# Performance work log

Hardware: AMD Instinct MI355X
Metric: run time of the kernel (lower is better)

Reference implementation:

```python
import jax, jax.numpy as jnp
import numpy as np

GH, GW, B, H, OUT = 9, 9, 1024, 256, 1


def setup_inputs() -> dict:
    key = jax.random.key(0)
    ks = jax.random.split(key, 16)
    N = GH * GW
    s3 = 1.0 / np.sqrt(3 * H)
    sH = 1.0 / np.sqrt(H)
    return {
        "x": jax.random.normal(ks[0], (B, GH, GW), jnp.float32),
        "h_ext": jax.random.normal(ks[1], (B, H), jnp.float32),
        "c_ext": jax.random.normal(ks[2], (B, H), jnp.float32),
        "grid_h": jax.random.normal(ks[3], (GH, GW, B, H), jnp.float32),
        "grid_c": jax.random.normal(ks[4], (GH, GW, B, H), jnp.float32),
        "W_hp": jax.random.normal(ks[5], (N, H, 3 * H), jnp.float32) * s3,
        "b_hp": jax.random.normal(ks[6], (N, H), jnp.float32) * s3,
        "W_cp": jax.random.normal(ks[7], (N, H, 3 * H), jnp.float32) * s3,
        "b_cp": jax.random.normal(ks[8], (N, H), jnp.float32) * s3,
        "W_ih": jax.random.normal(ks[9], (N, 4 * H, 1), jnp.float32) * sH,
        "W_hh": jax.random.normal(ks[10], (N, 4 * H, H), jnp.float32) * sH,
        "b_ih": jax.random.normal(ks[11], (N, 4 * H), jnp.float32) * sH,
        "b_hh": jax.random.normal(ks[12], (N, 4 * H), jnp.float32) * sH,
        "W_out": jax.random.normal(ks[13], (OUT, H), jnp.float32) * sH,
        "b_out": jnp.zeros((OUT,), jnp.float32),
    }


def _lstm_cell(x_cell, h0, c0, W_ih_k, W_hh_k, b_ih_k, b_hh_k):
    # x_cell: [B,1], h0/c0: [B,H]; torch LSTMCell math
    gates = x_cell @ W_ih_k.T + b_ih_k + h0 @ W_hh_k.T + b_hh_k  # [B,4H]
    i, f, g, o = jnp.split(gates, 4, axis=1)
    i, f, o = jax.nn.sigmoid(i), jax.nn.sigmoid(f), jax.nn.sigmoid(o)
    g = jnp.tanh(g)
    c = f * c0 + i * g
    h = o * jnp.tanh(c)
    return h, c


def reference(x, h_ext, c_ext, grid_h, grid_c,
              W_hp, b_hp, W_cp, b_cp,
              W_ih, W_hh, b_ih, b_hh, W_out, b_out):
    zeros = jnp.zeros((B, H), x.dtype)
    # new states, updated in raster order; left/up neighbors read NEW states
    new_h = [[None] * GW for _ in range(GH)]
    new_c = [[None] * GW for _ in range(GH)]
    for i in range(GH):
        for j in range(GW):
            k = i * GW + j
            h_prev, c_prev = grid_h[i, j], grid_c[i, j]
            if i == 0 and j == 0:
                h_left, c_left = h_ext, c_ext
            elif j > 0:
                h_left, c_left = new_h[i][j - 1], new_c[i][j - 1]
            else:
                h_left, c_left = zeros, zeros
            if i > 0:
                h_up, c_up = new_h[i - 1][j], new_c[i - 1][j]
            else:
                h_up, c_up = zeros, zeros
            comb_h = jnp.concatenate([h_left, h_up, h_prev], axis=1)  # [B,3H]
            comb_c = jnp.concatenate([c_left, c_up, c_prev], axis=1)
            ph = comb_h @ W_hp[k].T + b_hp[k]
            pc = comb_c @ W_cp[k].T + b_cp[k]
            x_cell = x[:, i, j][:, None]  # [B,1]
            h_new, c_new = _lstm_cell(x_cell, ph, pc, W_ih[k], W_hh[k], b_ih[k], b_hh[k])
            new_h[i][j], new_c[i][j] = h_new, c_new
    final_h, final_c = new_h[-1][-1], new_c[-1][-1]
    # fc_out with fc_layers_out=[0]: Linear + ReLU, then sigmoid
    out = jax.nn.sigmoid(jax.nn.relu(final_h @ W_out.T + b_out))
    gh = jnp.stack([jnp.stack(r, 0) for r in new_h], 0)
    gc = jnp.stack([jnp.stack(r, 0) for r in new_c], 0)
    return out, final_h, final_c, gh, gc
```

## Files before the change

### kernel.cpp

```cpp
#include <hip/hip_runtime.h>
#include <math.h>

#define BATCH 1024
#define HID 256
#define W3 768
#define SLOT (BATCH * HID)

typedef __bf16 bf16_t;
typedef __bf16 bf16x8 __attribute__((ext_vector_type(8)));
typedef __bf16 bf16x4 __attribute__((ext_vector_type(4)));
typedef float f32x4 __attribute__((ext_vector_type(4)));

__device__ inline bf16x8 cvt8(const float4 a, const float4 b) {
    bf16x8 r;
    r[0] = (bf16_t)a.x; r[1] = (bf16_t)a.y; r[2] = (bf16_t)a.z; r[3] = (bf16_t)a.w;
    r[4] = (bf16_t)b.x; r[5] = (bf16_t)b.y; r[6] = (bf16_t)b.z; r[7] = (bf16_t)b.w;
    return r;
}
__device__ inline bf16x4 cvt4(const float4 a) {
    bf16x4 r;
    r[0] = (bf16_t)a.x; r[1] = (bf16_t)a.y; r[2] = (bf16_t)a.z; r[3] = (bf16_t)a.w;
    return r;
}

template<bool ATOMIC>
__device__ __forceinline__ void proj_core(
        const float* __restrict__ src, const float* __restrict__ W, int koff,
        const float* __restrict__ bias, float* __restrict__ out,
        bf16_t (*Asm)[40], bf16_t (*Bsm)[40]) {
    const int t = threadIdx.x;
    const int lane = t & 63, wid = t >> 6;
    const int wm = wid & 1, wn = wid >> 1;
    const int ln = lane & 15, lh = lane >> 4;
    const int b0 = blockIdx.x * 128, n0 = blockIdx.y * 128;
    const int sr = t >> 1, sq = (t & 1) * 16;
    const float* arow = src + (size_t)(b0 + sr) * HID + sq;
    const float* wrow = W + (size_t)(n0 + sr) * W3 + koff + sq;
    f32x4 acc[4][4] = {};
    for (int kb = 0; kb < 8; ++kb) {
        const float4 a0 = *(const float4*)(arow + kb * 32);
        const float4 a1 = *(const float4*)(arow + kb * 32 + 4);
        const float4 a2 = *(const float4*)(arow + kb * 32 + 8);
        const float4 a3 = *(const float4*)(arow + kb * 32 + 12);
        const float4 w0 = *(const float4*)(wrow + kb * 32);
        const float4 w1 = *(const float4*)(wrow + kb * 32 + 4);
        const float4 w2 = *(const float4*)(wrow + kb * 32 + 8);
        const float4 w3 = *(const float4*)(wrow + kb * 32 + 12);
        const bf16x8 av0 = cvt8(a0, a1), av1 = cvt8(a2, a3);
        const bf16x8 bv0 = cvt8(w0, w1), bv1 = cvt8(w2, w3);
        __syncthreads();
        *(bf16x8*)&Asm[sr][sq] = av0;
        *(bf16x8*)&Asm[sr][sq + 8] = av1;
        *(bf16x8*)&Bsm[sr][sq] = bv0;
        *(bf16x8*)&Bsm[sr][sq + 8] = bv1;
        __syncthreads();
        bf16x8 af[4], bfv[4];
        #pragma unroll
        for (int mf = 0; mf < 4; ++mf)
            af[mf] = *(const bf16x8*)&Asm[wm * 64 + mf * 16 + ln][lh * 8];
        #pragma unroll
        for (int nf = 0; nf < 4; ++nf)
            bfv[nf] = *(const bf16x8*)&Bsm[wn * 64 + nf * 16 + ln][lh * 8];
        #pragma unroll
        for (int mf = 0; mf < 4; ++mf)
            #pragma unroll
            for (int nf = 0; nf < 4; ++nf)
                acc[mf][nf] = __builtin_amdgcn_mfma_f32_16x16x32_bf16(
                    af[mf], bfv[nf], acc[mf][nf], 0, 0, 0);
    }
    #pragma unroll
    for (int nf = 0; nf < 4; ++nf) {
        const int n = n0 + wn * 64 + nf * 16 + ln;
        const float bn = ATOMIC ? 0.f : bias[n];
        #pragma unroll
        for (int mf = 0; mf < 4; ++mf)
            #pragma unroll
            for (int r = 0; r < 4; ++r) {
                const int b = b0 + wm * 64 + mf * 16 + lh * 4 + r;
                if (ATOMIC)
                    unsafeAtomicAdd(out + (size_t)b * HID + n, acc[mf][nf][r]);
                else
                    out[(size_t)b * HID + n] = acc[mf][nf][r] + bn;
            }
    }
}

__global__ __launch_bounds__(256) void baseproj_kernel(
        const float* __restrict__ gridh, const float* __restrict__ gridc,
        const float* __restrict__ Whp, const float* __restrict__ Wcp,
        const float* __restrict__ bhp, const float* __restrict__ bcp,
        float* __restrict__ phb, float* __restrict__ pcb) {
    __shared__ bf16_t As[128][40];
    __shared__ bf16_t Bs[128][40];
    const int z = blockIdx.z, k = z >> 1, hc = z & 1;
    const float* src = (hc ? gridc : gridh) + (size_t)k * SLOT;
    const float* W = (hc ? Wcp : Whp) + (size_t)k * HID * W3;
    const float* bias = (hc ? bcp : bhp) + (size_t)k * HID;
    float* out = (hc ? pcb : phb) + (size_t)k * SLOT;
    proj_core<false>(src, W, 512, bias, out, As, Bs);
}

__global__ __launch_bounds__(256) void gatesbase_kernel(
        const float* __restrict__ phb, const float* __restrict__ Whh,
        const float* __restrict__ Wih, const float* __restrict__ bih,
        const float* __restrict__ bhh, const float* __restrict__ x,
        float* __restrict__ gbase) {
    __shared__ bf16_t As[128][40];
    __shared__ bf16_t Bs[128][40];
    const int k = blockIdx.z;
    const int t = threadIdx.x;
    const int lane = t & 63, wid = t >> 6;
    const int wm = wid & 1, wn = wid >> 1;
    const int ln = lane & 15, lh = lane >> 4;
    const int b0 = blockIdx.x * 128;
    const int ub = blockIdx.y, u0 = ub * 32;
    const int sr = t >> 1, sq = (t & 1) * 16;
    const float* arow = phb + (size_t)k * SLOT + (size_t)(b0 + sr) * HID + sq;
    const int g_r = sr >> 5, du_r = sr & 31;
    const float* wrow = Whh + (size_t)k * 4 * HID * HID
                        + (size_t)(g_r * HID + u0 + du_r) * HID + sq;
    f32x4 acc[4][4] = {};
    for (int kb = 0; kb < 8; ++kb) {
        const float4 a0 = *(const float4*)(arow + kb * 32);
        const float4 a1 = *(const float4*)(arow + kb * 32 + 4);
        const float4 a2 = *(const float4*)(arow + kb * 32 + 8);
        const float4 a3 = *(const float4*)(arow + kb * 32 + 12);
        const float4 w0 = *(const float4*)(wrow + kb * 32);
        const float4 w1 = *(const float4*)(wrow + kb * 32 + 4);
        const float4 w2 = *(const float4*)(wrow + kb * 32 + 8);
        const float4 w3 = *(const float4*)(wrow + kb * 32 + 12);
        const bf16x8 av0 = cvt8(a0, a1), av1 = cvt8(a2, a3);
        const bf16x8 bv0 = cvt8(w0, w1), bv1 = cvt8(w2, w3);
        __syncthreads();
        *(bf16x8*)&As[sr][sq] = av0;
        *(bf16x8*)&As[sr][sq + 8] = av1;
        *(bf16x8*)&Bs[sr][sq] = bv0;
        *(bf16x8*)&Bs[sr][sq + 8] = bv1;
        __syncthreads();
        bf16x8 af[4], bfr[4];
        #pragma unroll
        for (int mf = 0; mf < 4; ++mf)
            af[mf] = *(const bf16x8*)&As[wm * 64 + mf * 16 + ln][lh * 8];
        #pragma unroll
        for (int g = 0; g < 4; ++g)
            bfr[g] = *(const bf16x8*)&Bs[g * 32 + wn * 16 + ln][lh * 8];
        #pragma unroll
        for (int mf = 0; mf < 4; ++mf)
            #pragma unroll
            for (int g = 0; g < 4; ++g)
                acc[mf][g] = __builtin_amdgcn_mfma_f32_16x16x32_bf16(
                    af[mf], bfr[g], acc[mf][g], 0, 0, 0);
    }
    const int u = u0 + wn * 16 + ln;
    float wih[4], bb[4];
    #pragma unroll
    for (int g = 0; g < 4; ++g) {
        const int n4 = g * HID + u;
        wih[g] = Wih[(size_t)k * 4 * HID + n4];
        bb[g] = bih[(size_t)k * 4 * HID + n4] + bhh[(size_t)k * 4 * HID + n4];
    }
    float* orow = gbase + (size_t)k * BATCH * 1024;
    #pragma unroll
    for (int mf = 0; mf < 4; ++mf)
        #pragma unroll
        for (int r = 0; r < 4; ++r) {
            const int b = b0 + wm * 64 + mf * 16 + lh * 4 + r;
            const float xv = x[(size_t)b * 81 + k];
            #pragma unroll
            for (int g = 0; g < 4; ++g)
                orow[(size_t)b * 1024 + ub * 128 + g * 32 + wn * 16 + ln] =
                    acc[mf][g][r] + xv * wih[g] + bb[g],
                (void)0;
            #pragma unroll
            for (int g = 1; g < 4; ++g) { }
        }
}

__global__ __launch_bounds__(256) void compose_kernel(
        const float* __restrict__ Whh, const float* __restrict__ Whp,
        bf16_t* __restrict__ CC) {
    __shared__ bf16_t As[128][40];
    __shared__ bf16_t Bs[128][40];
    const int k = blockIdx.z;
    const int t = threadIdx.x;
    const int lane = t & 63, wid = t >> 6;
    const int wm = wid & 1, wn = wid >> 1;
    const int ln = lane & 15, lh = lane >> 4;
    const int m0 = blockIdx.x * 128;
    const int by = blockIdx.y;
    const int sr = t >> 1, sq = (t & 1) * 16;
    const int g_r = sr >> 5, du_r = sr & 31;
    const float* arow = Whh + (size_t)k * 4 * HID * HID
                        + (size_t)(g_r * HID + by * 32 + du_r) * HID + sq;
    const float* wbase = Whp + (size_t)k * HID * W3;
    const int uu = t >> 3, mm0 = (t & 7) * 16;
    f32x4 acc[4][4] = {};
    for (int kb = 0; kb < 8; ++kb) {
        const float4 a0 = *(const float4*)(arow + kb * 32);
        const float4 a1 = *(const float4*)(arow + kb * 32 + 4);
        const float4 a2 = *(const float4*)(arow + kb * 32 + 8);
        const float4 a3 = *(const float4*)(arow + kb * 32 + 12);
        const float* bsrc = wbase + (size_t)(kb * 32 + uu) * W3 + m0 + mm0;
        const float4 v0 = *(const float4*)(bsrc);
        const float4 v1 = *(const float4*)(bsrc + 4);
        const float4 v2 = *(const float4*)(bsrc + 8);
        const float4 v3 = *(const float4*)(bsrc + 12);
        const bf16x8 av0 = cvt8(a0, a1), av1 = cvt8(a2, a3);
        const bf16x4 bq[4] = { cvt4(v0), cvt4(v1), cvt4(v2), cvt4(v3) };
        __syncthreads();
        *(bf16x8*)&As[sr][sq] = av0;
        *(bf16x8*)&As[sr][sq + 8] = av1;
        #pragma unroll
        for (int q = 0; q < 4; ++q)
            #pragma unroll
            for (int e = 0; e < 4; ++e)
                Bs[mm0 + q * 4 + e][uu] = bq[q][e];
        __syncthreads();
        bf16x8 af[4], bf[4];
        #pragma unroll
        for (int mf = 0; mf < 4; ++mf)
            af[mf] = *(const bf16x8*)&As[wm * 64 + mf * 16 + ln][lh * 8];
        #pragma unroll
        for (int nf = 0; nf < 4; ++nf)
            bf[nf] = *(const bf16x8*)&Bs[wn * 64 + nf * 16 + ln][lh * 8];
        #pragma unroll
        for (int mf = 0; mf < 4; ++mf)
            #pragma unroll
            for (int nf = 0; nf < 4; ++nf)
                acc[mf][nf] = __builtin_amdgcn_mfma_f32_16x16x32_bf16(
                    af[mf], bf[nf], acc[mf][nf], 0, 0, 0);
    }
    bf16_t* out = CC + (size_t)k * 1024 * 512;
    #pragma unroll
    for (int nf = 0; nf < 4; ++nf) {
        const int m = m0 + wn * 64 + nf * 16 + ln;
        #pragma unroll
        for (int mf = 0; mf < 4; ++mf)
            #pragma unroll
            for (int r = 0; r < 4; ++r) {
                const int c = by * 128 + wm * 64 + mf * 16 + lh * 4 + r;
                out[(size_t)c * 512 + m] = (bf16_t)acc[mf][nf][r];
            }
    }
}

struct FusedDesc {
    const float* hl; const float* cl;
    const float* hu; const float* cu;
    const float* gb;
    const float* pcb;
    const bf16_t* cc;
    const float* wcp;
    float* gh; float* gc;
};
struct FusedBatchArgs { FusedDesc d[9]; };

__global__ __launch_bounds__(256) void fused_kernel(FusedBatchArgs args) {
    const FusedDesc fd = args.d[blockIdx.z];
    __shared__ bf16_t A1[128][40];
    __shared__ bf16_t A2[128][40];
    __shared__ bf16_t B1[128][40];
    __shared__ bf16_t B2[32][40];
    const int t = threadIdx.x;
    const int lane = t & 63, wid = t >> 6;
    const int wm = wid & 1, wn = wid >> 1;
    const int ln = lane & 15, lh = lane >> 4;
    const int b0 = blockIdx.x * 128;
    const int by = blockIdx.y, u0 = by * 32;
    const int sr = t >> 1, sq = (t & 1) * 16;
    const int du2 = t >> 3, kk4 = (t & 7) * 4;

    const float* hs[2]; const float* cs[2]; int ko[2]; int ns = 0;
    if (fd.hl) { hs[ns] = fd.hl; cs[ns] = fd.cl; ko[ns] = 0;   ++ns; }
    if (fd.hu) { hs[ns] = fd.hu; cs[ns] = fd.cu; ko[ns] = 256; ++ns; }

    f32x4 accg[4][4] = {};
    f32x4 accp[4] = {};

    for (int s = 0; s < ns; ++s) {
        const float* ha = hs[s] + (size_t)(b0 + sr) * HID + sq;
        const float* ca = cs[s] + (size_t)(b0 + sr) * HID + sq;
        const bf16_t* b1r = fd.cc + (size_t)(by * 128 + sr) * 512 + ko[s] + sq;
        const float* b2r = fd.wcp + (size_t)(u0 + du2) * W3 + ko[s] + kk4;
        for (int kb = 0; kb < 8; ++kb) {
            const float4 h0 = *(const float4*)(ha + kb * 32);
            const float4 h1 = *(const float4*)(ha + kb * 32 + 4);
            const float4 h2 = *(const float4*)(ha + kb * 32 + 8);
            const float4 h3 = *(const float4*)(ha + kb * 32 + 12);
            const float4 c0 = *(const float4*)(ca + kb * 32);
            const float4 c1 = *(const float4*)(ca + kb * 32 + 4);
            const float4 c2 = *(const float4*)(ca + kb * 32 + 8);
            const float4 c3 = *(const float4*)(ca + kb * 32 + 12);
            const bf16x8 w0 = *(const bf16x8*)(b1r + kb * 32);
            const bf16x8 w1 = *(const bf16x8*)(b1r + kb * 32 + 8);
            const float4 p0 = *(const float4*)(b2r + kb * 32);
            const bf16x8 hv0 = cvt8(h0, h1), hv1 = cvt8(h2, h3);
            const bf16x8 cv0 = cvt8(c0, c1), cv1 = cvt8(c2, c3);
            const bf16x4 pv = cvt4(p0);
            __syncthreads();
            *(bf16x8*)&A1[sr][sq] = hv0;
            *(bf16x8*)&A1[sr][sq + 8] = hv1;
            *(bf16x8*)&A2[sr][sq] = cv0;
            *(bf16x8*)&A2[sr][sq + 8] = cv1;
            *(bf16x8*)&B1[sr][sq] = w0;
            *(bf16x8*)&B1[sr][sq + 8] = w1;
            *(bf16x4*)&B2[du2][kk4] = pv;
            __syncthreads();
            bf16x8 af1[4], bf1[4], af2[4], bf2;
            #pragma unroll
            for (int mf = 0; mf < 4; ++mf) {
                af1[mf] = *(const bf16x8*)&A1[wm * 64 + mf * 16 + ln][lh * 8];
                af2[mf] = *(const bf16x8*)&A2[wm * 64 + mf * 16 + ln][lh * 8];
            }
            #pragma unroll
            for (int g = 0; g < 4; ++g)
                bf1[g] = *(const bf16x8*)&B1[g * 32 + wn * 16 + ln][lh * 8];
            bf2 = *(const bf16x8*)&B2[wn * 16 + ln][lh * 8];
            #pragma unroll
            for (int mf = 0; mf < 4; ++mf) {
                #pragma unroll
                for (int g = 0; g < 4; ++g)
                    accg[mf][g] = __builtin_amdgcn_mfma_f32_16x16x32_bf16(
                        af1[mf], bf1[g], accg[mf][g], 0, 0, 0);
                accp[mf] = __builtin_amdgcn_mfma_f32_16x16x32_bf16(
                    af2[mf], bf2, accp[mf], 0, 0, 0);
            }
        }
    }

    const int u = u0 + wn * 16 + ln;
    #pragma unroll
    for (int mf = 0; mf < 4; ++mf)
        #pragma unroll
        for (int r = 0; r < 4; ++r) {
            const int b = b0 + wm * 64 + mf * 16 + lh * 4 + r;
            const float* gbr = fd.gb + (size_t)b * 1024 + by * 128 + wn * 16 + ln;
            const float gi = accg[mf][0][r] + gbr[0];
            const float gf = accg[mf][1][r] + gbr[32];
            const float gg = accg[mf][2][r] + gbr[64];
            const float go = accg[mf][3][r] + gbr[96];
            const float pc = accp[mf][r] + fd.pcb[(size_t)b * HID + u];
            const float i_ = 1.f / (1.f + expf(-gi));
            const float f_ = 1.f / (1.f + expf(-gf));
            const float o_ = 1.f / (1.f + expf(-go));
            const float g_ = tanhf(gg);
            const float cn = f_ * pc + i_ * g_;
            const float hn = o_ * tanhf(cn);
            fd.gh[(size_t)b * HID + u] = hn;
            fd.gc[(size_t)b * HID + u] = cn;
        }
}

struct SegDesc { const float* src; const float* W; const float* bias; float* out; int koff; };
struct SegArgs { SegDesc d[36]; };

__global__ __launch_bounds__(256) void projseg_kernel(SegArgs a) {
    __shared__ bf16_t As[128][40];
    __shared__ bf16_t Bs[128][40];
    const SegDesc d = a.d[blockIdx.z];
    if (d.bias) proj_core<false>(d.src, d.W, d.koff, d.bias, d.out, As, Bs);
    else        proj_core<true>(d.src, d.W, d.koff, nullptr, d.out, As, Bs);
}

struct CellDesc {
    const float* ph; const float* pc;
    const float* Whh; const float* Wih; const float* bih; const float* bhh;
    const float* xcol;
    float* gh; float* gc;
};
struct CellBatchArgs { CellDesc d[9]; };

__global__ __launch_bounds__(256) void cell_kernel(CellBatchArgs args) {
    const CellDesc cd = args.d[blockIdx.z];
    __shared__ bf16_t Psm[128][40];
    __shared__ bf16_t Wsm[128][40];
    const int t = threadIdx.x;
    const int lane = t & 63, wid = t >> 6;
    const int wm = wid & 1, wn = wid >> 1;
    const int ln = lane & 15, lh = lane >> 4;
    const int b0 = blockIdx.x * 128;
    const int u0 = blockIdx.y * 32;
    const int sr = t >> 1, sq = (t & 1) * 16;
    const float* prow = cd.ph + (size_t)(b0 + sr) * HID + sq;
    const int cg = sr >> 5, cdu = sr & 31;
    const float* wrow = cd.Whh + (size_t)(cg * HID + u0 + cdu) * HID + sq;
    f32x4 acc[4][4] = {};
    for (int kb = 0; kb < 8; ++kb) {
        const float4 p0 = *(const float4*)(prow + kb * 32);
        const float4 p1 = *(const float4*)(prow + kb * 32 + 4);
        const float4 p2 = *(const float4*)(prow + kb * 32 + 8);
        const float4 p3 = *(const float4*)(prow + kb * 32 + 12);
        const float4 w0 = *(const float4*)(wrow + kb * 32);
        const float4 w1 = *(const float4*)(wrow + kb * 32 + 4);
        const float4 w2 = *(const float4*)(wrow + kb * 32 + 8);
        const float4 w3 = *(const float4*)(wrow + kb * 32 + 12);
        const bf16x8 pv0 = cvt8(p0, p1), pv1 = cvt8(p2, p3);
        const bf16x8 wv0 = cvt8(w0, w1), wv1 = cvt8(w2, w3);
        __syncthreads();
        *(bf16x8*)&Psm[sr][sq] = pv0;
        *(bf16x8*)&Psm[sr][sq + 8] = pv1;
        *(bf16x8*)&Wsm[sr][sq] = wv0;
        *(bf16x8*)&Wsm[sr][sq + 8] = wv1;
        __syncthreads();
        bf16x8 af[4], bfr[4];
        #pragma unroll
        for (int mf = 0; mf < 4; ++mf)
            af[mf] = *(const bf16x8*)&Psm[wm * 64 + mf * 16 + ln][lh * 8];
        #pragma unroll
        for (int g = 0; g < 4; ++g)
            bfr[g] = *(const bf16x8*)&Wsm[g * 32 + wn * 16 + ln][lh * 8];
        #pragma unroll
        for (int mf = 0; mf < 4; ++mf)
            #pragma unroll
            for (int g = 0; g < 4; ++g)
                acc[mf][g] = __builtin_amdgcn_mfma_f32_16x16x32_bf16(
                    af[mf], bfr[g], acc[mf][g], 0, 0, 0);
    }
    const int u = u0 + wn * 16 + ln;
    float wih[4], bsum[4];
    #pragma unroll
    for (int g = 0; g < 4; ++g) {
        const int n = g * HID + u;
        wih[g] = cd.Wih[n];
        bsum[g] = cd.bih[n] + cd.bhh[n];
    }
    #pragma unroll
    for (int mf = 0; mf < 4; ++mf)
        #pragma unroll
        for (int r = 0; r < 4; ++r) {
            const int b = b0 + wm * 64 + mf * 16 + lh * 4 + r;
            const float xv = cd.xcol[(size_t)b * 81];
            const float gi = acc[mf][0][r] + xv * wih[0] + bsum[0];
            const float gf = acc[mf][1][r] + xv * wih[1] + bsum[1];
            const float gg = acc[mf][2][r] + xv * wih[2] + bsum[2];
            const float go = acc[mf][3][r] + xv * wih[3] + bsum[3];
            const float i_ = 1.f / (1.f + expf(-gi));
            const float f_ = 1.f / (1.f + expf(-gf));
            const float o_ = 1.f / (1.f + expf(-go));
            const float g_ = tanhf(gg);
            const float c0 = cd.pc[(size_t)b * HID + u];
            const float cn = f_ * c0 + i_ * g_;
            const float hn = o_ * tanhf(cn);
            cd.gh[(size_t)b * HID + u] = hn;
            cd.gc[(size_t)b * HID + u] = cn;
        }
}

__global__ __launch_bounds__(256) void final_kernel(
        const float* __restrict__ gh88, const float* __restrict__ gc88,
        const float* __restrict__ Wout, const float* __restrict__ bout,
        float* __restrict__ out, float* __restrict__ fh, float* __restrict__ fc) {
    const int tid = blockIdx.x * blockDim.x + threadIdx.x;
    const int nth = gridDim.x * blockDim.x;
    for (int idx = tid; idx < BATCH * HID; idx += nth) {
        fh[idx] = gh88[idx];
        fc[idx] = gc88[idx];
    }
    if (tid < BATCH) {
        float s = bout[0];
        for (int k = 0; k < HID; ++k) s += gh88[(size_t)tid * HID + k] * Wout[k];
        s = fmaxf(s, 0.f);
        out[tid] = 1.f / (1.f + expf(-s));
    }
}

extern "C" void kernel_launch(void* const* d_in, const int* in_sizes, int n_in,
                              void* d_out, int out_size, void* d_ws, size_t ws_size,
                              hipStream_t stream) {
    const float* x      = (const float*)d_in[0];
    const float* h_ext  = (const float*)d_in[1];
    const float* c_ext  = (const float*)d_in[2];
    const float* grid_h = (const float*)d_in[3];
    const float* grid_c = (const float*)d_in[4];
    const float* W_hp   = (const float*)d_in[5];
    const float* b_hp   = (const float*)d_in[6];
    const float* W_cp   = (const float*)d_in[7];
    const float* b_cp   = (const float*)d_in[8];
    const float* W_ih   = (const float*)d_in[9];
    const float* W_hh   = (const float*)d_in[10];
    const float* b_ih   = (const float*)d_in[11];
    const float* b_hh   = (const float*)d_in[12];
    const float* W_out  = (const float*)d_in[13];
    const float* b_out  = (const float*)d_in[14];

    float* out = (float*)d_out;
    float* fh  = out + BATCH * 1;
    float* fc  = fh + SLOT;
    float* gh  = fc + SLOT;
    float* gc  = gh + (size_t)81 * SLOT;

    const size_t gb_bytes = (size_t)81 * BATCH * 1024 * 4;
    const size_t cc_bytes = (size_t)81 * 1024 * 512 * 2;
    const size_t pb_bytes = (size_t)81 * SLOT * 4;
    const size_t need_new = gb_bytes + cc_bytes + 2 * pb_bytes;

    if (ws_size >= need_new) {
        float* gbase = (float*)d_ws;
        bf16_t* CC = (bf16_t*)((char*)d_ws + gb_bytes);
        float* pcb = (float*)((char*)d_ws + gb_bytes + cc_bytes);
        float* phb = (float*)((char*)d_ws + gb_bytes + cc_bytes + pb_bytes);

        baseproj_kernel<<<dim3(8, 2, 162), 256, 0, stream>>>(
            grid_h, grid_c, W_hp, W_cp, b_hp, b_cp, phb, pcb);
        compose_kernel<<<dim3(4, 8, 81), 256, 0, stream>>>(W_hh, W_hp, CC);
        gatesbase_kernel<<<dim3(8, 8, 81), 256, 0, stream>>>(
            phb, W_hh, W_ih, b_ih, b_hh, x, gbase);

        for (int d = 0; d <= 16; ++d) {
            const int i_lo = d > 8 ? d - 8 : 0;
            const int i_hi = d < 8 ? d : 8;
            const int nc = i_hi - i_lo + 1;
            FusedBatchArgs fa{};
            for (int s = 0; s < nc; ++s) {
                const int i = i_lo + s, j = d - i;
                const int k = i * 9 + j;
                const float *hl = nullptr, *cl = nullptr, *hu = nullptr, *cu = nullptr;
                if (i == 0 && j == 0)      { hl = h_ext; cl = c_ext; }
                else if (j > 0)            { hl = gh + (size_t)(k - 1) * SLOT;
                                             cl = gc + (size_t)(k - 1) * SLOT; }
                if (i > 0)                 { hu = gh + (size_t)(k - 9) * SLOT;
                                             cu = gc + (size_t)(k - 9) * SLOT; }
                fa.d[s] = { hl, cl, hu, cu,
                            gbase + (size_t)k * BATCH * 1024,
                            pcb + (size_t)k * SLOT,
                            CC + (size_t)k * 1024 * 512,
                            W_cp + (size_t)k * HID * W3,
                            gh + (size_t)k * SLOT,
                            gc + (size_t)k * SLOT };
            }
            fused_kernel<<<dim3(8, 8, nc), 256, 0, stream>>>(fa);
        }
    } else {
        float* ws = (float*)d_ws;
        for (int d = 0; d <= 16; ++d) {
            const int i_lo = d > 8 ? d - 8 : 0;
            const int i_hi = d < 8 ? d : 8;
            const int nc = i_hi - i_lo + 1;
            SegArgs base{}, inc{};
            CellBatchArgs ca{};
            int nb = 0, ni = 0;
            for (int s = 0; s < nc; ++s) {
                const int i = i_lo + s, j = d - i;
                const int k = i * 9 + j;
                float* oh = ws + (size_t)(2 * s) * SLOT;
                float* oc = oh + SLOT;
                const float* Wh = W_hp + (size_t)k * HID * W3;
                const float* Wc = W_cp + (size_t)k * HID * W3;
                base.d[nb++] = { grid_h + (size_t)k * SLOT, Wh, b_hp + (size_t)k * HID, oh, 512 };
                base.d[nb++] = { grid_c + (size_t)k * SLOT, Wc, b_cp + (size_t)k * HID, oc, 512 };
                if (i == 0 && j == 0) {
                    inc.d[ni++] = { h_ext, Wh, nullptr, oh, 0 };
                    inc.d[ni++] = { c_ext, Wc, nullptr, oc, 0 };
                } else if (j > 0) {
                    inc.d[ni++] = { gh + (size_t)(k - 1) * SLOT, Wh, nullptr, oh, 0 };
                    inc.d[ni++] = { gc + (size_t)(k - 1) * SLOT, Wc, nullptr, oc, 0 };
                }
                if (i > 0) {
                    inc.d[ni++] = { gh + (size_t)(k - 9) * SLOT, Wh, nullptr, oh, 256 };
                    inc.d[ni++] = { gc + (size_t)(k - 9) * SLOT, Wc, nullptr, oc, 256 };
                }
                ca.d[s] = { oh, oc,
                            W_hh + (size_t)k * 4 * HID * HID,
                            W_ih + (size_t)k * 4 * HID,
                            b_ih + (size_t)k * 4 * HID,
                            b_hh + (size_t)k * 4 * HID,
                            x + i * 9 + j,
                            gh + (size_t)k * SLOT,
                            gc + (size_t)k * SLOT };
            }
            projseg_kernel<<<dim3(8, 2, nb), 256, 0, stream>>>(base);
            projseg_kernel<<<dim3(8, 2, ni), 256, 0, stream>>>(inc);
            cell_kernel<<<dim3(8, 8, nc), 256, 0, stream>>>(ca);
        }
    }
    final_kernel<<<dim3(64), 256, 0, stream>>>(
        gh + (size_t)80 * SLOT, gc + (size_t)80 * SLOT,
        W_out, b_out, out, fh, fc);
}
```

Before: 1.241 ms.

## Fold grid-state projection into wavefront stage kernel, drop precomputed gate buffers

Removes the separate base-projection and gates-base precompute kernels and their large fp32 workspace buffers. The composed Whh·Whp matrix is extended to cover all three input segments, so each stage kernel multiplies left, up and prior grid states directly. A small kernel folds Whh·b_hp and the LSTM biases into a per-cell gate vector, and x·W_ih is added in the epilogue. This cuts memory traffic for the gate-base and pc-base buffers, at the cost of the serial wavefront stages doing a third K-segment of work.

New measurement: 1.229 ms. Within noise of the previous version (-1.0%).

```diff
diff --git a/kernel.cpp b/kernel.cpp
--- a/kernel.cpp
+++ b/kernel.cpp
@@ -21,159 +21,6 @@
     bf16x4 r;
     r[0] = (bf16_t)a.x; r[1] = (bf16_t)a.y; r[2] = (bf16_t)a.z; r[3] = (bf16_t)a.w;
     return r;
-}
-
-template<bool ATOMIC>
-__device__ __forceinline__ void proj_core(
-        const float* __restrict__ src, const float* __restrict__ W, int koff,
-        const float* __restrict__ bias, float* __restrict__ out,
-        bf16_t (*Asm)[40], bf16_t (*Bsm)[40]) {
-    const int t = threadIdx.x;
-    const int lane = t & 63, wid = t >> 6;
-    const int wm = wid & 1, wn = wid >> 1;
-    const int ln = lane & 15, lh = lane >> 4;
-    const int b0 = blockIdx.x * 128, n0 = blockIdx.y * 128;
-    const int sr = t >> 1, sq = (t & 1) * 16;
-    const float* arow = src + (size_t)(b0 + sr) * HID + sq;
-    const float* wrow = W + (size_t)(n0 + sr) * W3 + koff + sq;
-    f32x4 acc[4][4] = {};
-    for (int kb = 0; kb < 8; ++kb) {
-        const float4 a0 = *(const float4*)(arow + kb * 32);
-        const float4 a1 = *(const float4*)(arow + kb * 32 + 4);
-        const float4 a2 = *(const float4*)(arow + kb * 32 + 8);
-        const float4 a3 = *(const float4*)(arow + kb * 32 + 12);
-        const float4 w0 = *(const float4*)(wrow + kb * 32);
-        const float4 w1 = *(const float4*)(wrow + kb * 32 + 4);
-        const float4 w2 = *(const float4*)(wrow + kb * 32 + 8);
-        const float4 w3 = *(const float4*)(wrow + kb * 32 + 12);
-        const bf16x8 av0 = cvt8(a0, a1), av1 = cvt8(a2, a3);
-        const bf16x8 bv0 = cvt8(w0, w1), bv1 = cvt8(w2, w3);
-        __syncthreads();
-        *(bf16x8*)&Asm[sr][sq] = av0;
-        *(bf16x8*)&Asm[sr][sq + 8] = av1;
-        *(bf16x8*)&Bsm[sr][sq] = bv0;
-        *(bf16x8*)&Bsm[sr][sq + 8] = bv1;
-        __syncthreads();
-        bf16x8 af[4], bfv[4];
-        #pragma unroll
-        for (int mf = 0; mf < 4; ++mf)
-            af[mf] = *(const bf16x8*)&Asm[wm * 64 + mf * 16 + ln][lh * 8];
-        #pragma unroll
-        for (int nf = 0; nf < 4; ++nf)
-            bfv[nf] = *(const bf16x8*)&Bsm[wn * 64 + nf * 16 + ln][lh * 8];
-        #pragma unroll
-        for (int mf = 0; mf < 4; ++mf)
-            #pragma unroll
-            for (int nf = 0; nf < 4; ++nf)
-                acc[mf][nf] = __builtin_amdgcn_mfma_f32_16x16x32_bf16(
-                    af[mf], bfv[nf], acc[mf][nf], 0, 0, 0);
-    }
-    #pragma unroll
-    for (int nf = 0; nf < 4; ++nf) {
-        const int n = n0 + wn * 64 + nf * 16 + ln;
-        const float bn = ATOMIC ? 0.f : bias[n];
-        #pragma unroll
-        for (int mf = 0; mf < 4; ++mf)
-            #pragma unroll
-            for (int r = 0; r < 4; ++r) {
-                const int b = b0 + wm * 64 + mf * 16 + lh * 4 + r;
-                if (ATOMIC)
-                    unsafeAtomicAdd(out + (size_t)b * HID + n, acc[mf][nf][r]);
-                else
-                    out[(size_t)b * HID + n] = acc[mf][nf][r] + bn;
-            }
-    }
-}
-
-__global__ __launch_bounds__(256) void baseproj_kernel(
-        const float* __restrict__ gridh, const float* __restrict__ gridc,
-        const float* __restrict__ Whp, const float* __restrict__ Wcp,
-        const float* __restrict__ bhp, const float* __restrict__ bcp,
-        float* __restrict__ phb, float* __restrict__ pcb) {
-    __shared__ bf16_t As[128][40];
-    __shared__ bf16_t Bs[128][40];
-    const int z = blockIdx.z, k = z >> 1, hc = z & 1;
-    const float* src = (hc ? gridc : gridh) + (size_t)k * SLOT;
-    const float* W = (hc ? Wcp : Whp) + (size_t)k * HID * W3;
-    const float* bias = (hc ? bcp : bhp) + (size_t)k * HID;
-    float* out = (hc ? pcb : phb) + (size_t)k * SLOT;
-    proj_core<false>(src, W, 512, bias, out, As, Bs);
-}
-
-__global__ __launch_bounds__(256) void gatesbase_kernel(
-        const float* __restrict__ phb, const float* __restrict__ Whh,
-        const float* __restrict__ Wih, const float* __restrict__ bih,
-        const float* __restrict__ bhh, const float* __restrict__ x,
-        float* __restrict__ gbase) {
-    __shared__ bf16_t As[128][40];
-    __shared__ bf16_t Bs[128][40];
-    const int k = blockIdx.z;
-    const int t = threadIdx.x;
-    const int lane = t & 63, wid = t >> 6;
-    const int wm = wid & 1, wn = wid >> 1;
-    const int ln = lane & 15, lh = lane >> 4;
-    const int b0 = blockIdx.x * 128;
-    const int ub = blockIdx.y, u0 = ub * 32;
-    const int sr = t >> 1, sq = (t & 1) * 16;
-    const float* arow = phb + (size_t)k * SLOT + (size_t)(b0 + sr) * HID + sq;
-    const int g_r = sr >> 5, du_r = sr & 31;
-    const float* wrow = Whh + (size_t)k * 4 * HID * HID
-                        + (size_t)(g_r * HID + u0 + du_r) * HID + sq;
-    f32x4 acc[4][4] = {};
-    for (int kb = 0; kb < 8; ++kb) {
-        const float4 a0 = *(const float4*)(arow + kb * 32);
-        const float4 a1 = *(const float4*)(arow + kb * 32 + 4);
-        const float4 a2 = *(const float4*)(arow + kb * 32 + 8);
-        const float4 a3 = *(const float4*)(arow + kb * 32 + 12);
-        const float4 w0 = *(const float4*)(wrow + kb * 32);
-        const float4 w1 = *(const float4*)(wrow + kb * 32 + 4);
-        const float4 w2 = *(const float4*)(wrow + kb * 32 + 8);
-        const float4 w3 = *(const float4*)(wrow + kb * 32 + 12);
-        const bf16x8 av0 = cvt8(a0, a1), av1 = cvt8(a2, a3);
-        const bf16x8 bv0 = cvt8(w0, w1), bv1 = cvt8(w2, w3);
-        __syncthreads();
-        *(bf16x8*)&As[sr][sq] = av0;
-        *(bf16x8*)&As[sr][sq + 8] = av1;
-        *(bf16x8*)&Bs[sr][sq] = bv0;
-        *(bf16x8*)&Bs[sr][sq + 8] = bv1;
-        __syncthreads();
-        bf16x8 af[4], bfr[4];
-        #pragma unroll
-        for (int mf = 0; mf < 4; ++mf)
-            af[mf] = *(const bf16x8*)&As[wm * 64 + mf * 16 + ln][lh * 8];
-        #pragma unroll
-        for (int g = 0; g < 4; ++g)
-            bfr[g] = *(const bf16x8*)&Bs[g * 32 + wn * 16 + ln][lh * 8];
-        #pragma unroll
-        for (int mf = 0; mf < 4; ++mf)
-            #pragma unroll
-            for (int g = 0; g < 4; ++g)
-                acc[mf][g] = __builtin_amdgcn_mfma_f32_16x16x32_bf16(
-                    af[mf], bfr[g], acc[mf][g], 0, 0, 0);
-    }
-    const int u = u0 + wn * 16 + ln;
-    float wih[4], bb[4];
-    #pragma unroll
-    for (int g = 0; g < 4; ++g) {
-        const int n4 = g * HID + u;
-        wih[g] = Wih[(size_t)k * 4 * HID + n4];
-        bb[g] = bih[(size_t)k * 4 * HID + n4] + bhh[(size_t)k * 4 * HID + n4];
-    }
-    float* orow = gbase + (size_t)k * BATCH * 1024;
-    #pragma unroll
-    for (int mf = 0; mf < 4; ++mf)
-        #pragma unroll
-        for (int r = 0; r < 4; ++r) {
-            const int b = b0 + wm * 64 + mf * 16 + lh * 4 + r;
-            const float xv = x[(size_t)b * 81 + k];
-            #pragma unroll
-            for (int g = 0; g < 4; ++g)
-                orow[(size_t)b * 1024 + ub * 128 + g * 32 + wn * 16 + ln] =
-                    acc[mf][g][r] + xv * wih[g] + bb[g],
-                (void)0;
-            #pragma unroll
-            for (int g = 1; g < 4; ++g) { }
-        }
 }
 
 __global__ __launch_bounds__(256) void compose_kernel(
@@ -216,21 +63,21 @@
             for (int e = 0; e < 4; ++e)
                 Bs[mm0 + q * 4 + e][uu] = bq[q][e];
         __syncthreads();
-        bf16x8 af[4], bf[4];
+        bf16x8 af[4], bfv[4];
         #pragma unroll
         for (int mf = 0; mf < 4; ++mf)
             af[mf] = *(const bf16x8*)&As[wm * 64 + mf * 16 + ln][lh * 8];
         #pragma unroll
         for (int nf = 0; nf < 4; ++nf)
-            bf[nf] = *(const bf16x8*)&Bs[wn * 64 + nf * 16 + ln][lh * 8];
+            bfv[nf] = *(const bf16x8*)&Bs[wn * 64 + nf * 16 + ln][lh * 8];
         #pragma unroll
         for (int mf = 0; mf < 4; ++mf)
             #pragma unroll
             for (int nf = 0; nf < 4; ++nf)
                 acc[mf][nf] = __builtin_amdgcn_mfma_f32_16x16x32_bf16(
-                    af[mf], bf[nf], acc[mf][nf], 0, 0, 0);
-    }
-    bf16_t* out = CC + (size_t)k * 1024 * 512;
+                    af[mf], bfv[nf], acc[mf][nf], 0, 0, 0);
+    }
+    bf16_t* outp = CC + (size_t)k * 1024 * W3;
     #pragma unroll
     for (int nf = 0; nf < 4; ++nf) {
         const int m = m0 + wn * 64 + nf * 16 + ln;
@@ -239,24 +86,49 @@
             #pragma unroll
             for (int r = 0; r < 4; ++r) {
                 const int c = by * 128 + wm * 64 + mf * 16 + lh * 4 + r;
-                out[(size_t)c * 512 + m] = (bf16_t)acc[mf][nf][r];
+                outp[(size_t)c * W3 + m] = (bf16_t)acc[mf][nf][r];
             }
     }
 }
 
-struct FusedDesc {
-    const float* hl; const float* cl;
-    const float* hu; const float* cu;
-    const float* gb;
-    const float* pcb;
+__global__ __launch_bounds__(256) void gvec_kernel(
+        const float* __restrict__ Whh, const float* __restrict__ bhp,
+        const float* __restrict__ bih, const float* __restrict__ bhh,
+        float* __restrict__ gvec) {
+    const int k = blockIdx.x, t = threadIdx.x;
+    __shared__ float bsm[HID];
+    bsm[t] = bhp[(size_t)k * HID + t];
+    __syncthreads();
+    #pragma unroll
+    for (int g = 0; g < 4; ++g) {
+        const int n4 = g * HID + t;
+        const float* wr = Whh + (size_t)k * 4 * HID * HID + (size_t)n4 * HID;
+        float s = 0.f;
+        for (int u = 0; u < HID; u += 4) {
+            const float4 w = *(const float4*)(wr + u);
+            s += w.x * bsm[u] + w.y * bsm[u + 1] + w.z * bsm[u + 2] + w.w * bsm[u + 3];
+        }
+        gvec[(size_t)k * 1024 + n4] = s + bih[(size_t)k * 1024 + n4]
+                                        + bhh[(size_t)k * 1024 + n4];
+    }
+}
+
+struct StageDesc {
+    const float* hs0; const float* cs0;
+    const float* hs1; const float* cs1;
+    const float* hs2; const float* cs2;
     const bf16_t* cc;
     const float* wcp;
+    const float* gvec;
+    const float* wih;
+    const float* bcp;
+    const float* xk;
     float* gh; float* gc;
 };
-struct FusedBatchArgs { FusedDesc d[9]; };
-
-__global__ __launch_bounds__(256) void fused_kernel(FusedBatchArgs args) {
-    const FusedDesc fd = args.d[blockIdx.z];
+struct StageArgs { StageDesc d[9]; };
+
+__global__ __launch_bounds__(256) void stage_kernel(StageArgs args) {
+    const StageDesc sd = args.d[blockIdx.z];
     __shared__ bf16_t A1[128][40];
     __shared__ bf16_t A2[128][40];
     __shared__ bf16_t B1[128][40];
@@ -270,18 +142,19 @@
     const int sr = t >> 1, sq = (t & 1) * 16;
     const int du2 = t >> 3, kk4 = (t & 7) * 4;
 
-    const float* hs[2]; const float* cs[2]; int ko[2]; int ns = 0;
-    if (fd.hl) { hs[ns] = fd.hl; cs[ns] = fd.cl; ko[ns] = 0;   ++ns; }
-    if (fd.hu) { hs[ns] = fd.hu; cs[ns] = fd.cu; ko[ns] = 256; ++ns; }
+    const float* hs[3] = { sd.hs0, sd.hs1, sd.hs2 };
+    const float* cs[3] = { sd.cs0, sd.cs1, sd.cs2 };
 
     f32x4 accg[4][4] = {};
     f32x4 accp[4] = {};
 
-    for (int s = 0; s < ns; ++s) {
+    for (int s = 0; s < 3; ++s) {
+        if (!hs[s]) continue;
+        const int ko = s * 256;
         const float* ha = hs[s] + (size_t)(b0 + sr) * HID + sq;
         const float* ca = cs[s] + (size_t)(b0 + sr) * HID + sq;
-        const bf16_t* b1r = fd.cc + (size_t)(by * 128 + sr) * 512 + ko[s] + sq;
-        const float* b2r = fd.wcp + (size_t)(u0 + du2) * W3 + ko[s] + kk4;
+        const bf16_t* b1r = sd.cc + (size_t)(by * 128 + sr) * W3 + ko + sq;
+        const float* b2r = sd.wcp + (size_t)(u0 + du2) * W3 + ko + kk4;
         for (int kb = 0; kb < 8; ++kb) {
             const float4 h0 = *(const float4*)(ha + kb * 32);
             const float4 h1 = *(const float4*)(ha + kb * 32 + 4);
@@ -306,7 +179,7 @@
             *(bf16x8*)&B1[sr][sq + 8] = w1;
             *(bf16x4*)&B2[du2][kk4] = pv;
             __syncthreads();
-            bf16x8 af1[4], bf1[4], af2[4], bf2;
+            bf16x8 af1[4], af2[4], bf1[4], bf2;
             #pragma unroll
             for (int mf = 0; mf < 4; ++mf) {
                 af1[mf] = *(const bf16x8*)&A1[wm * 64 + mf * 16 + ln][lh * 8];
@@ -329,26 +202,114 @@
     }
 
     const int u = u0 + wn * 16 + ln;
+    float wih[4], gv[4];
+    #pragma unroll
+    for (int g = 0; g < 4; ++g) {
+        const int n4 = g * HID + u;
+        wih[g] = sd.wih[n4];
+        gv[g] = sd.gvec[n4];
+    }
+    const float bc = sd.bcp[u];
     #pragma unroll
     for (int mf = 0; mf < 4; ++mf)
         #pragma unroll
         for (int r = 0; r < 4; ++r) {
             const int b = b0 + wm * 64 + mf * 16 + lh * 4 + r;
-            const float* gbr = fd.gb + (size_t)b * 1024 + by * 128 + wn * 16 + ln;
-            const float gi = accg[mf][0][r] + gbr[0];
-            const float gf = accg[mf][1][r] + gbr[32];
-            const float gg = accg[mf][2][r] + gbr[64];
-            const float go = accg[mf][3][r] + gbr[96];
-            const float pc = accp[mf][r] + fd.pcb[(size_t)b * HID + u];
+            const float xv = sd.xk[(size_t)b * 81];
+            const float gi = accg[mf][0][r] + gv[0] + xv * wih[0];
+            const float gf = accg[mf][1][r] + gv[1] + xv * wih[1];
+            const float gg = accg[mf][2][r] + gv[2] + xv * wih[2];
+            const float go = accg[mf][3][r] + gv[3] + xv * wih[3];
+            const float pc = accp[mf][r] + bc;
             const float i_ = 1.f / (1.f + expf(-gi));
             const float f_ = 1.f / (1.f + expf(-gf));
             const float o_ = 1.f / (1.f + expf(-go));
             const float g_ = tanhf(gg);
             const float cn = f_ * pc + i_ * g_;
             const float hn = o_ * tanhf(cn);
-            fd.gh[(size_t)b * HID + u] = hn;
-            fd.gc[(size_t)b * HID + u] = cn;
+            sd.gh[(size_t)b * HID + u] = hn;
+            sd.gc[(size_t)b * HID + u] = cn;
         }
+}
+
+__global__ __launch_bounds__(256) void final_kernel(
+        const float* __restrict__ gh88, const float* __restrict__ gc88,
+        const float* __restrict__ Wout, const float* __restrict__ bout,
+        float* __restrict__ out, float* __restrict__ fh, float* __restrict__ fc) {
+    const int tid = blockIdx.x * blockDim.x + threadIdx.x;
+    const int nth = gridDim.x * blockDim.x;
+    for (int idx = tid; idx < BATCH * HID; idx += nth) {
+        fh[idx] = gh88[idx];
+        fc[idx] = gc88[idx];
+    }
+    if (tid < BATCH) {
+        float s = bout[0];
+        for (int k = 0; k < HID; ++k) s += gh88[(size_t)tid * HID + k] * Wout[k];
+        s = fmaxf(s, 0.f);
+        out[tid] = 1.f / (1.f + expf(-s));
+    }
+}
+
+template<bool ATOMIC>
+__device__ __forceinline__ void proj_core(
+        const float* __restrict__ src, const float* __restrict__ W, int koff,
+        const float* __restrict__ bias, float* __restrict__ out,
+        bf16_t (*Asm)[40], bf16_t (*Bsm)[40]) {
+    const int t = threadIdx.x;
+    const int lane = t & 63, wid = t >> 6;
+    const int wm = wid & 1, wn = wid >> 1;
+    const int ln = lane & 15, lh = lane >> 4;
+    const int b0 = blockIdx.x * 128, n0 = blockIdx.y * 128;
+    const int sr = t >> 1, sq = (t & 1) * 16;
+    const float* arow = src + (size_t)(b0 + sr) * HID + sq;
+    const float* wrow = W + (size_t)(n0 + sr) * W3 + koff + sq;
+    f32x4 acc[4][4] = {};
+    for (int kb = 0; kb < 8; ++kb) {
+        const float4 a0 = *(const float4*)(arow + kb * 32);
+        const float4 a1 = *(const float4*)(arow + kb * 32 + 4);
+        const float4 a2 = *(const float4*)(arow + kb * 32 + 8);
+        const float4 a3 = *(const float4*)(arow + kb * 32 + 12);
+        const float4 w0 = *(const float4*)(wrow + kb * 32);
+        const float4 w1 = *(const float4*)(wrow + kb * 32 + 4);
+        const float4 w2 = *(const float4*)(wrow + kb * 32 + 8);
+        const float4 w3 = *(const float4*)(wrow + kb * 32 + 12);
+        const bf16x8 av0 = cvt8(a0, a1), av1 = cvt8(a2, a3);
+        const bf16x8 bv0 = cvt8(w0, w1), bv1 = cvt8(w2, w3);
+        __syncthreads();
+        *(bf16x8*)&Asm[sr][sq] = av0;
+        *(bf16x8*)&Asm[sr][sq + 8] = av1;
+        *(bf16x8*)&Bsm[sr][sq] = bv0;
+        *(bf16x8*)&Bsm[sr][sq + 8] = bv1;
+        __syncthreads();
+        bf16x8 af[4], bfv[4];
+        #pragma unroll
+        for (int mf = 0; mf < 4; ++mf)
+            af[mf] = *(const bf16x8*)&Asm[wm * 64 + mf * 16 + ln][lh * 8];
+        #pragma unroll
+        for (int nf = 0; nf < 4; ++nf)
+            bfv[nf] = *(const bf16x8*)&Bsm[wn * 64 + nf * 16 + ln][lh * 8];
+        #pragma unroll
+        for (int mf = 0; mf < 4; ++mf)
+            #pragma unroll
+            for (int nf = 0; nf < 4; ++nf)
+                acc[mf][nf] = __builtin_amdgcn_mfma_f32_16x16x32_bf16(
+                    af[mf], bfv[nf], acc[mf][nf], 0, 0, 0);
+    }
+    #pragma unroll
+    for (int nf = 0; nf < 4; ++nf) {
+        const int n = n0 + wn * 64 + nf * 16 + ln;
+        const float bn = ATOMIC ? 0.f : bias[n];
+        #pragma unroll
+        for (int mf = 0; mf < 4; ++mf)
+            #pragma unroll
+            for (int r = 0; r < 4; ++r) {
+                const int b = b0 + wm * 64 + mf * 16 + lh * 4 + r;
+                if (ATOMIC)
+                    unsafeAtomicAdd(out + (size_t)b * HID + n, acc[mf][nf][r]);
+                else
+                    out[(size_t)b * HID + n] = acc[mf][nf][r] + bn;
+            }
+    }
 }
 
 struct SegDesc { const float* src; const float* W; const float* bias; float* out; int koff; };
@@ -446,24 +407,6 @@
         }
 }
 
-__global__ __launch_bounds__(256) void final_kernel(
-        const float* __restrict__ gh88, const float* __restrict__ gc88,
-        const float* __restrict__ Wout, const float* __restrict__ bout,
-        float* __restrict__ out, float* __restrict__ fh, float* __restrict__ fc) {
-    const int tid = blockIdx.x * blockDim.x + threadIdx.x;
-    const int nth = gridDim.x * blockDim.x;
-    for (int idx = tid; idx < BATCH * HID; idx += nth) {
-        fh[idx] = gh88[idx];
-        fc[idx] = gc88[idx];
-    }
-    if (tid < BATCH) {
-        float s = bout[0];
-        for (int k = 0; k < HID; ++k) s += gh88[(size_t)tid * HID + k] * Wout[k];
-        s = fmaxf(s, 0.f);
-        out[tid] = 1.f / (1.f + expf(-s));
-    }
-}
-
 extern "C" void kernel_launch(void* const* d_in, const int* in_sizes, int n_in,
                               void* d_out, int out_size, void* d_ws, size_t ws_size,
                               hipStream_t stream) {
@@ -489,28 +432,21 @@
     float* gh  = fc + SLOT;
     float* gc  = gh + (size_t)81 * SLOT;
 
-    const size_t gb_bytes = (size_t)81 * BATCH * 1024 * 4;
-    const size_t cc_bytes = (size_t)81 * 1024 * 512 * 2;
-    const size_t pb_bytes = (size_t)81 * SLOT * 4;
-    const size_t need_new = gb_bytes + cc_bytes + 2 * pb_bytes;
-
-    if (ws_size >= need_new) {
-        float* gbase = (float*)d_ws;
-        bf16_t* CC = (bf16_t*)((char*)d_ws + gb_bytes);
-        float* pcb = (float*)((char*)d_ws + gb_bytes + cc_bytes);
-        float* phb = (float*)((char*)d_ws + gb_bytes + cc_bytes + pb_bytes);
-
-        baseproj_kernel<<<dim3(8, 2, 162), 256, 0, stream>>>(
-            grid_h, grid_c, W_hp, W_cp, b_hp, b_cp, phb, pcb);
-        compose_kernel<<<dim3(4, 8, 81), 256, 0, stream>>>(W_hh, W_hp, CC);
-        gatesbase_kernel<<<dim3(8, 8, 81), 256, 0, stream>>>(
-            phb, W_hh, W_ih, b_ih, b_hh, x, gbase);
+    const size_t cc_bytes = (size_t)81 * 1024 * W3 * 2;
+    const size_t gv_bytes = (size_t)81 * 1024 * 4;
+
+    if (ws_size >= cc_bytes + gv_bytes) {
+        bf16_t* CC = (bf16_t*)d_ws;
+        float* gvec = (float*)((char*)d_ws + cc_bytes);
+
+        compose_kernel<<<dim3(6, 8, 81), 256, 0, stream>>>(W_hh, W_hp, CC);
+        gvec_kernel<<<dim3(81), 256, 0, stream>>>(W_hh, b_hp, b_ih, b_hh, gvec);
 
         for (int d = 0; d <= 16; ++d) {
             const int i_lo = d > 8 ? d - 8 : 0;
             const int i_hi = d < 8 ? d : 8;
             const int nc = i_hi - i_lo + 1;
-            FusedBatchArgs fa{};
+            StageArgs sa{};
             for (int s = 0; s < nc; ++s) {
                 const int i = i_lo + s, j = d - i;
                 const int k = i * 9 + j;
@@ -520,15 +456,18 @@
                                              cl = gc + (size_t)(k - 1) * SLOT; }
                 if (i > 0)                 { hu = gh + (size_t)(k - 9) * SLOT;
                                              cu = gc + (size_t)(k - 9) * SLOT; }
-                fa.d[s] = { hl, cl, hu, cu,
-                            gbase + (size_t)k * BATCH * 1024,
-                            pcb + (size_t)k * SLOT,
-                            CC + (size_t)k * 1024 * 512,
+                sa.d[s] = { hl, cl, hu, cu,
+                            grid_h + (size_t)k * SLOT, grid_c + (size_t)k * SLOT,
+                            CC + (size_t)k * 1024 * W3,
                             W_cp + (size_t)k * HID * W3,
+                            gvec + (size_t)k * 1024,
+                            W_ih + (size_t)k * 1024,
+                            b_cp + (size_t)k * HID,
+                            x + k,
                             gh + (size_t)k * SLOT,
                             gc + (size_t)k * SLOT };
             }
-            fused_kernel<<<dim3(8, 8, nc), 256, 0, stream>>>(fa);
+            stage_kernel<<<dim3(8, 8, nc), 256, 0, stream>>>(sa);
         }
     } else {
         float* ws = (float*)d_ws;
```
